# Optimization experiments

Measured on AMD Instinct MI355X. Metric: run time of the kernel, lower is better.

Reference implementation:

```python
import jax, jax.numpy as jnp
import numpy as np

D_MODEL, D_STATE, D_CONV, EXPAND = 1024, 16, 4, 2
D_INNER = D_MODEL * EXPAND
BATCH, SEQ = 2, 2048


def setup_inputs() -> dict:
    key = jax.random.key(0)
    ks = jax.random.split(key, 10)
    s = lambda d: 1.0 / np.sqrt(d)
    return {
        "x": jax.random.normal(ks[0], (BATCH, SEQ, D_MODEL), jnp.float32),
        "norm_w": jnp.ones((D_MODEL,), jnp.float32),
        "norm_b": jnp.zeros((D_MODEL,), jnp.float32),
        "W_in": jax.random.normal(ks[1], (2 * D_INNER, D_MODEL), jnp.float32) * s(D_MODEL),
        "conv_w": jax.random.normal(ks[2], (D_INNER, D_CONV), jnp.float32) * s(D_CONV),
        "conv_b": jnp.zeros((D_INNER,), jnp.float32),
        "W_dt": jax.random.normal(ks[3], (D_INNER, D_INNER), jnp.float32) * s(D_INNER),
        "b_dt": jnp.zeros((D_INNER,), jnp.float32),
        "W_B": jax.random.normal(ks[4], (D_STATE, D_INNER), jnp.float32) * s(D_INNER),
        "W_C": jax.random.normal(ks[5], (D_STATE, D_INNER), jnp.float32) * s(D_INNER),
        "D": jnp.ones((D_INNER,), jnp.float32),
        "A_log": jnp.broadcast_to(jnp.log(jnp.arange(1, D_STATE + 1, dtype=jnp.float32)), (D_INNER, D_STATE)),
        "W_out": jax.random.normal(ks[6], (D_MODEL, D_INNER), jnp.float32) * s(D_INNER),
    }


def _layernorm(x, w, b, eps=1e-5):
    mu = jnp.mean(x, axis=-1, keepdims=True)
    var = jnp.var(x, axis=-1, keepdims=True)
    return (x - mu) * jax.lax.rsqrt(var + eps) * w + b


def _causal_depthwise_conv(x, w, b):
    # x: [B, L, C], w: [C, K], b: [C]; torch Conv1d(padding=K-1) then slice [:L] == left-pad causal conv
    K = w.shape[1]
    xp = jnp.pad(x, ((0, 0), (K - 1, 0), (0, 0)))
    L = x.shape[1]
    out = b
    for k in range(K):  # small fixed K=4
        out = out + xp[:, k:k + L, :] * w[:, k]
    return out


def reference(x, norm_w, norm_b, W_in, conv_w, conv_b, W_dt, b_dt, W_B, W_C, D, A_log, W_out):
    residual = x
    xn = _layernorm(x, norm_w, norm_b)
    xz = jnp.einsum("bld,ed->ble", xn, W_in)            # [B,L,2*d_inner]
    x_part, z = jnp.split(xz, 2, axis=-1)
    x_conv = jax.nn.silu(_causal_depthwise_conv(x_part, conv_w, conv_b))  # [B,L,di]
    dt = jax.nn.softplus(jnp.einsum("bld,ed->ble", x_conv, W_dt) + b_dt)  # [B,L,di]
    Bm = jnp.einsum("bld,nd->bln", x_conv, W_B)         # [B,L,ds]
    Cm = jnp.einsum("bld,nd->bln", x_conv, W_C)         # [B,L,ds]
    A = -jnp.exp(A_log)                                  # [di,ds]

    def step(h, inp):
        dt_t, B_t, C_t, xc_t = inp                       # [B,di],[B,ds],[B,ds],[B,di]
        h = h * jnp.exp(A[None] * dt_t[:, :, None]) + xc_t[:, :, None] * B_t[:, None, :] * dt_t[:, :, None]
        y_t = jnp.sum(h * C_t[:, None, :], axis=-1)      # [B,di]
        return h, y_t

    h0 = jnp.zeros((x.shape[0], A.shape[0], A.shape[1]), x_conv.dtype)
    # scan over time: move L to leading axis
    xs = (jnp.swapaxes(dt, 0, 1), jnp.swapaxes(Bm, 0, 1), jnp.swapaxes(Cm, 0, 1), jnp.swapaxes(x_conv, 0, 1))
    _, y = jax.lax.scan(step, h0, xs)                    # y: [L,B,di]
    y = jnp.swapaxes(y, 0, 1)
    y = y + x_conv * D
    y = y * jax.nn.silu(z)
    return residual + jnp.einsum("ble,de->bld", y, W_out)
```

## Files before the change

kernel.cpp:

```cpp
#include <hip/hip_runtime.h>
#include <cstdint>
#include <cstddef>

#define D_MODEL 1024
#define D_INNER 2048
#define D_STATE 16
#define SEQ     2048
#define NROWS   4096

typedef short short4v __attribute__((ext_vector_type(4)));
typedef short short8v __attribute__((ext_vector_type(8)));
typedef float float4v __attribute__((ext_vector_type(4)));

__device__ __forceinline__ float bf2f(short u) {
  union { unsigned int i; float f; } v;
  v.i = ((unsigned int)(unsigned short)u) << 16;
  return v.f;
}
__device__ __forceinline__ short f2bf(float f) {
  union { float f; unsigned int i; } v; v.f = f;
  unsigned int r = v.i + 0x7FFFu + ((v.i >> 16) & 1u);
  return (short)(r >> 16);
}
__device__ __forceinline__ float lde(const void* p, size_t i, int f32) {
  return f32 ? ((const float*)p)[i] : bf2f(((const short*)p)[i]);
}
__device__ __forceinline__ void async16(short* lds, const short* g) {
  __builtin_amdgcn_global_load_lds(
      (const __attribute__((address_space(1))) unsigned int*)g,
      (__attribute__((address_space(3))) unsigned int*)lds, 16, 0, 0);
}

__global__ __launch_bounds__(64) void probe_kernel(const unsigned int* __restrict__ xw,
                                                   int* __restrict__ flag) {
  int cnt = 0;
  for (int i = threadIdx.x; i < 1024; i += 64) {
    unsigned e = (xw[i] >> 7) & 0xFFu;
    cnt += (e >= 100u && e <= 150u) ? 1 : 0;
  }
  #pragma unroll
  for (int o = 32; o >= 1; o >>= 1) cnt += __shfl_xor(cnt, o);
  if (threadIdx.x == 0) *flag = (cnt < 614) ? 1 : 0;
}

#define WIN_N  4194304u
#define WDT_N  4194304u
#define WBC_N  32768u
#define WPAD_N 196608u
#define WCAT_N (WDT_N + 2u*WBC_N + WPAD_N)
#define WOUT_N 2097152u
__global__ __launch_bounds__(256) void cvt_kernel(
    const void* __restrict__ Win, const void* __restrict__ Wdt,
    const void* __restrict__ WBp, const void* __restrict__ WCp,
    const void* __restrict__ Wout, short* __restrict__ dst,
    const int* __restrict__ flag) {
  const int f32 = *flag;
  const size_t i = ((size_t)blockIdx.x * 256 + threadIdx.x) * 8;
  const void* src = nullptr; size_t off = 0; bool zero = false;
  if (i < WIN_N) { src = Win; off = i; }
  else {
    size_t j = i - WIN_N;
    if (j < WDT_N) { src = Wdt; off = j; }
    else {
      j -= WDT_N;
      if (j < WBC_N) { src = WBp; off = j; }
      else {
        j -= WBC_N;
        if (j < WBC_N) { src = WCp; off = j; }
        else {
          j -= WBC_N;
          if (j < WPAD_N) zero = true;
          else { src = Wout; off = j - WPAD_N; }
        }
      }
    }
  }
  short8v o;
  if (zero) {
    #pragma unroll
    for (int j = 0; j < 8; ++j) o[j] = 0;
  } else if (f32) {
    const float* s = (const float*)src + off;
    #pragma unroll
    for (int j = 0; j < 8; ++j) o[j] = f2bf(s[j]);
  } else {
    o = *(const short8v*)((const short*)src + off);
  }
  *(short8v*)&dst[i] = o;
}

__global__ __launch_bounds__(256) void ln_kernel(
    const void* __restrict__ x, const void* __restrict__ w,
    const void* __restrict__ bb, short* __restrict__ xn,
    const int* __restrict__ flag) {
  const int f32 = *flag;
  const int row = blockIdx.x;
  const int tid = threadIdx.x;
  float v0, v1, v2, v3;
  if (f32) {
    float4v xv = ((const float4v*)((const float*)x + (size_t)row * D_MODEL))[tid];
    v0 = xv[0]; v1 = xv[1]; v2 = xv[2]; v3 = xv[3];
  } else {
    short4v xv = *(const short4v*)&((const short*)x)[(size_t)row * D_MODEL + tid * 4];
    v0 = bf2f(xv[0]); v1 = bf2f(xv[1]); v2 = bf2f(xv[2]); v3 = bf2f(xv[3]);
  }
  float s = v0 + v1 + v2 + v3;
  float q = v0*v0 + v1*v1 + v2*v2 + v3*v3;
  #pragma unroll
  for (int off = 32; off >= 1; off >>= 1) {
    s += __shfl_xor(s, off);
    q += __shfl_xor(q, off);
  }
  __shared__ float red[8];
  const int wid = tid >> 6;
  if ((tid & 63) == 0) { red[wid] = s; red[4 + wid] = q; }
  __syncthreads();
  s = red[0] + red[1] + red[2] + red[3];
  q = red[4] + red[5] + red[6] + red[7];
  const float mu = s * (1.f / 1024.f);
  const float var = q * (1.f / 1024.f) - mu * mu;
  const float rstd = rsqrtf(var + 1e-5f);
  short4v ov;
  #pragma unroll
  for (int j = 0; j < 4; ++j) {
    const float vj = (j == 0) ? v0 : (j == 1) ? v1 : (j == 2) ? v2 : v3;
    const float o = (vj - mu) * rstd * lde(w, tid * 4 + j, f32) + lde(bb, tid * 4 + j, f32);
    ov[j] = f2bf(o);
  }
  *(short4v*)&xn[(size_t)row * D_MODEL + tid * 4] = ov;
}

template <int MODE, int BM>
__global__ __launch_bounds__(2 * BM) void gemm_bt(
    const short* __restrict__ A, int lda, const short* __restrict__ B,
    void* __restrict__ Cv, int N, int K, const void* __restrict__ aux,
    float* __restrict__ Bmo, float* __restrict__ Cmo,
    const int* __restrict__ flag) {
  __shared__ __align__(16) short As0[BM * 32];
  __shared__ __align__(16) short As1[BM * 32];
  __shared__ __align__(16) short Bs0[128 * 32];
  __shared__ __align__(16) short Bs1[128 * 32];
  const int f32 = *flag;
  const int tid = threadIdx.x;
  const int bm = blockIdx.y * BM;
  const int bn = blockIdx.x << 7;
  const int wid = tid >> 6;
  const int lane = tid & 63;
  const int wm = (wid >> 1) << 6;
  const int wn = (wid & 1) << 6;

  float4v acc[4][4];
  #pragma unroll
  for (int i = 0; i < 4; ++i)
    #pragma unroll
    for (int j = 0; j < 4; ++j) acc[i][j] = (float4v){0.f, 0.f, 0.f, 0.f};

  const int srow = tid >> 2;
  const int scol = (((tid & 3) ^ ((tid >> 3) & 3)) << 3);
  const short* ga = A + (size_t)(bm + srow) * lda + scol;
  const short* gb = B + (size_t)(bn + srow) * K + scol;
  const size_t astep = (size_t)(BM / 2) * lda;
  const size_t bstep = (size_t)64 * K;

  const int fr = lane & 15;
  const int fq = (((lane >> 4) ^ ((lane >> 1) & 3)) << 3);

  constexpr int STAGE_DMAS = (BM == 256) ? 3 : 4;
  constexpr int VM_WAIT = 0x3FF0 | STAGE_DMAS;

#define STAGE(Ad, Bd, kk) do {                              \
    async16(&Ad[tid * 8], ga + (kk));                       \
    async16(&Ad[BM * 16 + tid * 8], ga + astep + (kk));     \
    if (BM == 256) {                                        \
      async16(&Bd[tid * 8], gb + (kk));                     \
    } else {                                                \
      async16(&Bd[tid * 8], gb + (kk));                     \
      async16(&Bd[2048 + tid * 8], gb + bstep + (kk));      \
    } } while (0)

  auto compute = [&](const short* Asrc, const short* Bsrc) {
    short8v af[4], bfv[4];
    #pragma unroll
    for (int i = 0; i < 4; ++i)
      af[i] = *(const short8v*)&Asrc[(wm + i * 16 + fr) * 32 + fq];
    #pragma unroll
    for (int j = 0; j < 4; ++j)
      bfv[j] = *(const short8v*)&Bsrc[(wn + j * 16 + fr) * 32 + fq];
    #pragma unroll
    for (int i = 0; i < 4; ++i)
      #pragma unroll
      for (int j = 0; j < 4; ++j)
        acc[i][j] = __builtin_amdgcn_mfma_f32_16x16x32_bf16(af[i], bfv[j], acc[i][j], 0, 0, 0);
  };

  const int nk = K >> 5;
  STAGE(As0, Bs0, 0);
  for (int k2 = 0; k2 < nk; k2 += 2) {
    STAGE(As1, Bs1, (k2 + 1) << 5);
    __builtin_amdgcn_s_waitcnt(VM_WAIT);
    __builtin_amdgcn_s_barrier();
    compute(As0, Bs0);
    __builtin_amdgcn_s_barrier();
    if (k2 + 2 < nk) {
      STAGE(As0, Bs0, (k2 + 2) << 5);
      __builtin_amdgcn_s_waitcnt(VM_WAIT);
    } else {
      __builtin_amdgcn_s_waitcnt(0x3FF0);
    }
    __builtin_amdgcn_s_barrier();
    compute(As1, Bs1);
    __builtin_amdgcn_s_barrier();
  }
#undef STAGE

  const int er = (lane >> 4) << 2;
  const int ec = lane & 15;
  #pragma unroll
  for (int i = 0; i < 4; ++i) {
    #pragma unroll
    for (int j = 0; j < 4; ++j) {
      const int gcol = bn + wn + j * 16 + ec;
      #pragma unroll
      for (int r = 0; r < 4; ++r) {
        const int grow = bm + wm + i * 16 + er + r;
        float v = acc[i][j][r];
        if (MODE == 1) {
          if (gcol < 2048) {
            v += lde(aux, gcol, f32);
            v = (v > 15.f) ? v : log1pf(__expf(v));
            ((short*)Cv)[(size_t)grow * 2048 + gcol] = f2bf(v);
          } else if (gcol < 2064) {
            Bmo[(size_t)grow * 16 + (gcol - 2048)] = v;
          } else if (gcol < 2080) {
            Cmo[(size_t)grow * 16 + (gcol - 2064)] = v;
          }
        } else {
          const size_t idx = (size_t)grow * N + gcol;
          if (MODE == 2) {
            v += lde(aux, idx, f32);
            if (f32) ((float*)Cv)[idx] = v;
            else     ((short*)Cv)[idx] = f2bf(v);
          } else {
            ((short*)Cv)[idx] = f2bf(v);
          }
        }
      }
    }
  }
}

__global__ __launch_bounds__(256) void bc_kernel(
    const short* __restrict__ xcv, const short* __restrict__ wbc,
    float* __restrict__ Bmo, float* __restrict__ Cmo) {
  const int tid = threadIdx.x;
  const int w = tid >> 6;
  const int lane = tid & 63;
  const int fr = lane & 15;
  const int hi = lane >> 4;
  const int r0 = blockIdx.x << 4;
  const short* ap  = xcv + (size_t)(r0 + fr) * 2048 + hi * 8;
  const short* b0p = wbc + (size_t)fr * 2048 + hi * 8;
  const short* b1p = wbc + (size_t)(16 + fr) * 2048 + hi * 8;
  float4v acc0 = (float4v){0.f, 0.f, 0.f, 0.f};
  float4v acc1 = (float4v){0.f, 0.f, 0.f, 0.f};
  #pragma unroll 4
  for (int k = w * 32; k < 2048; k += 128) {
    const short8v af  = *(const short8v*)(ap + k);
    const short8v bf0 = *(const short8v*)(b0p + k);
    const short8v bf1 = *(const short8v*)(b1p + k);
    acc0 = __builtin_amdgcn_mfma_f32_16x16x32_bf16(af, bf0, acc0, 0, 0, 0);
    acc1 = __builtin_amdgcn_mfma_f32_16x16x32_bf16(af, bf1, acc1, 0, 0, 0);
  }
  __shared__ float red[3][64][8];
  if (w) {
    #pragma unroll
    for (int r = 0; r < 4; ++r) {
      red[w - 1][lane][r]     = acc0[r];
      red[w - 1][lane][4 + r] = acc1[r];
    }
  }
  __syncthreads();
  if (w == 0) {
    #pragma unroll
    for (int c = 0; c < 3; ++c)
      #pragma unroll
      for (int r = 0; r < 4; ++r) {
        acc0[r] += red[c][lane][r];
        acc1[r] += red[c][lane][4 + r];
      }
    const int er = hi << 2;
    const int ec = fr;
    #pragma unroll
    for (int r = 0; r < 4; ++r) {
      Bmo[(size_t)(r0 + er + r) * 16 + ec] = acc0[r];
      Cmo[(size_t)(r0 + er + r) * 16 + ec] = acc1[r];
    }
  }
}

#define CONV_RPB 8
__global__ __launch_bounds__(256) void conv_silu(
    const short* __restrict__ xz, const void* __restrict__ cw,
    const void* __restrict__ cb, short* __restrict__ xc,
    const int* __restrict__ flag) {
  const int f32 = *flag;
  const int r0 = blockIdx.x * CONV_RPB;
  const int c0 = threadIdx.x << 3;
  const int t0 = r0 & (SEQ - 1);

  float wreg[32], bias[8];
  if (f32) {
    const float4v* wp = (const float4v*)((const float*)cw + (size_t)c0 * 4);
    #pragma unroll
    for (int q = 0; q < 8; ++q) {
      const float4v v = wp[q];
      #pragma unroll
      for (int k = 0; k < 4; ++k) wreg[q * 4 + k] = v[k];
    }
    const float4v* bp = (const float4v*)((const float*)cb + c0);
    const float4v b0 = bp[0], b1 = bp[1];
    #pragma unroll
    for (int j = 0; j < 4; ++j) { bias[j] = b0[j]; bias[4 + j] = b1[j]; }
  } else {
    const short8v* wp = (const short8v*)((const short*)cw + (size_t)c0 * 4);
    #pragma unroll
    for (int q = 0; q < 4; ++q) {
      const short8v v = wp[q];
      #pragma unroll
      for (int e = 0; e < 8; ++e) wreg[q * 8 + e] = bf2f(v[e]);
    }
    const short8v bv = *(const short8v*)((const short*)cb + c0);
    #pragma unroll
    for (int j = 0; j < 8; ++j) bias[j] = bf2f(bv[j]);
  }

  float xw[4][8];
  #pragma unroll
  for (int k = 0; k < 3; ++k) {
    if (t0 + k - 3 >= 0) {
      const short8v v = *(const short8v*)&xz[(size_t)(r0 + k - 3) * 4096 + c0];
      #pragma unroll
      for (int j = 0; j < 8; ++j) xw[k][j] = bf2f(v[j]);
    } else {
      #pragma unroll
      for (int j = 0; j < 8; ++j) xw[k][j] = 0.f;
    }
  }
  #pragma unroll
  for (int t = 0; t < CONV_RPB; ++t) {
    const int row = r0 + t;
    const short8v v = *(const short8v*)&xz[(size_t)row * 4096 + c0];
    #pragma unroll
    for (int j = 0; j < 8; ++j) xw[3][j] = bf2f(v[j]);
    short8v ov;
    #pragma unroll
    for (int j = 0; j < 8; ++j) {
      float a = bias[j];
      #pragma unroll
      for (int k = 0; k < 4; ++k) a += xw[k][j] * wreg[j * 4 + k];
      ov[j] = f2bf(a / (1.f + __expf(-a)));
    }
    *(short8v*)&xc[(size_t)row * D_INNER + c0] = ov;
    #pragma unroll
    for (int k = 0; k < 3; ++k)
      #pragma unroll
      for (int j = 0; j < 8; ++j) xw[k][j] = xw[k + 1][j];
  }
}

#define SCAN_CK 64
#define SCAN_ST 32
__global__ __launch_bounds__(1024, 4) void scan_kernel(
    const short* __restrict__ dtb, const short* __restrict__ xcv,
    const float* __restrict__ Bm, const float* __restrict__ Cm,
    short* __restrict__ xzb, const void* __restrict__ A_log,
    const void* __restrict__ Dv, const int* __restrict__ flag) {
  const int f32 = *flag;
  const int tid = threadIdx.x;
  const int dl = tid & 15;
  const int ck = tid >> 4;
  const int di = (blockIdx.x << 4) + dl;
  const int b = blockIdx.y;
  const int r0 = (b << 11) + ck * SCAN_ST;

  const short* dtp = dtb + (size_t)r0 * 2048 + di;
  const short* xcp = xcv + (size_t)r0 * 2048 + di;
  const float* bmp = Bm + (size_t)r0 * 16;
  const float* cmp = Cm + (size_t)r0 * 16;
  const short* zp = xzb + (size_t)r0 * 4096 + 2048 + di;
  short* yp = xzb + (size_t)r0 * 4096 + di;

  float Ac[16];
  #pragma unroll
  for (int s = 0; s < 16; ++s)
    Ac[s] = -__expf(lde(A_log, (size_t)di * 16 + s, f32));
  const float Dval = lde(Dv, di, f32);

  bool pat = true;
  #pragma unroll
  for (int s = 1; s < 16; ++s)
    pat = pat && (fabsf(Ac[s] - (float)(s + 1) * Ac[0]) <= fabsf(Ac[s]) * 1e-3f + 1e-6f);
  const float al = Ac[0] * 1.442695041f;

#define POWCHAIN(es, e1) do {                                        \
    es[0] = (e1);                                                    \
    es[1] = es[0] * es[0];  es[2] = es[1] * es[0];                   \
    es[3] = es[1] * es[1];  es[4] = es[3] * es[0];                   \
    es[5] = es[3] * es[1];  es[6] = es[3] * es[2];                   \
    es[7] = es[3] * es[3];  es[8] = es[7] * es[0];                   \
    es[9] = es[7] * es[1];  es[10] = es[7] * es[2];                  \
    es[11] = es[7] * es[3]; es[12] = es[7] * es[4];                  \
    es[13] = es[7] * es[5]; es[14] = es[7] * es[6];                  \
    es[15] = es[7] * es[7]; } while (0)

  float h[16];
  #pragma unroll
  for (int s = 0; s < 16; ++s) h[s] = 0.f;
  float sdt = 0.f;

  if (pat) {
    #pragma unroll 2
    for (int t = 0; t < SCAN_ST; ++t) {
      const float dt = bf2f(dtp[(size_t)t * 2048]);
      const float xc = bf2f(xcp[(size_t)t * 2048]);
      const float4v b0 = *(const float4v*)&bmp[t * 16];
      const float4v b1 = *(const float4v*)&bmp[t * 16 + 4];
      const float4v b2 = *(const float4v*)&bmp[t * 16 + 8];
      const float4v b3 = *(const float4v*)&bmp[t * 16 + 12];
      sdt += dt;
      const float u = xc * dt;
      float es[16];
      POWCHAIN(es, exp2f(al * dt));
      #pragma unroll
      for (int s = 0; s < 4; ++s) {
        h[s]      = h[s]      * es[s]      + u * b0[s];
        h[s + 4]  = h[s + 4]  * es[s + 4]  + u * b1[s];
        h[s + 8]  = h[s + 8]  * es[s + 8]  + u * b2[s];
        h[s + 12] = h[s + 12] * es[s + 12] + u * b3[s];
      }
    }
  } else {
    #pragma unroll 2
    for (int t = 0; t < SCAN_ST; ++t) {
      const float dt = bf2f(dtp[(size_t)t * 2048]);
      const float xc = bf2f(xcp[(size_t)t * 2048]);
      const float4v b0 = *(const float4v*)&bmp[t * 16];
      const float4v b1 = *(const float4v*)&bmp[t * 16 + 4];
      const float4v b2 = *(const float4v*)&bmp[t * 16 + 8];
      const float4v b3 = *(const float4v*)&bmp[t * 16 + 12];
      sdt += dt;
      const float u = xc * dt;
      #pragma unroll
      for (int s = 0; s < 4; ++s) {
        h[s]      = h[s]      * __expf(Ac[s]      * dt) + u * b0[s];
        h[s + 4]  = h[s + 4]  * __expf(Ac[s + 4]  * dt) + u * b1[s];
        h[s + 8]  = h[s + 8]  * __expf(Ac[s + 8]  * dt) + u * b2[s];
        h[s + 12] = h[s + 12] * __expf(Ac[s + 12] * dt) + u * b3[s];
      }
    }
  }

  __shared__ float sdt_s[SCAN_CK][16];
  __shared__ float hc_s[SCAN_CK][16][17];
  sdt_s[ck][dl] = sdt;
  #pragma unroll
  for (int s = 0; s < 16; ++s) hc_s[ck][dl][s] = h[s];
  __syncthreads();
  if (tid < 256) {
    const int s = tid >> 4;
    const float Acs = -__expf(lde(A_log, (size_t)di * 16 + s, f32));
    float hs = 0.f;
    #pragma unroll 4
    for (int c = 0; c < SCAN_CK; ++c) {
      const float hend = hc_s[c][dl][s];
      hc_s[c][dl][s] = hs;
      hs = __expf(Acs * sdt_s[c][dl]) * hs + hend;
    }
  }
  __syncthreads();
  #pragma unroll
  for (int s = 0; s < 16; ++s) h[s] = hc_s[ck][dl][s];

  if (pat) {
    #pragma unroll 2
    for (int t = 0; t < SCAN_ST; ++t) {
      const float dt = bf2f(dtp[(size_t)t * 2048]);
      const float xc = bf2f(xcp[(size_t)t * 2048]);
      const float4v b0 = *(const float4v*)&bmp[t * 16];
      const float4v b1 = *(const float4v*)&bmp[t * 16 + 4];
      const float4v b2 = *(const float4v*)&bmp[t * 16 + 8];
      const float4v b3 = *(const float4v*)&bmp[t * 16 + 12];
      const float4v c0 = *(const float4v*)&cmp[t * 16];
      const float4v c1 = *(const float4v*)&cmp[t * 16 + 4];
      const float4v c2 = *(const float4v*)&cmp[t * 16 + 8];
      const float4v c3 = *(const float4v*)&cmp[t * 16 + 12];
      const float u = xc * dt;
      float es[16];
      POWCHAIN(es, exp2f(al * dt));
      float p0 = 0.f, p1 = 0.f, p2 = 0.f, p3 = 0.f;
      #pragma unroll
      for (int s = 0; s < 4; ++s) {
        h[s]      = h[s]      * es[s]      + u * b0[s];
        h[s + 4]  = h[s + 4]  * es[s + 4]  + u * b1[s];
        h[s + 8]  = h[s + 8]  * es[s + 8]  + u * b2[s];
        h[s + 12] = h[s + 12] * es[s + 12] + u * b3[s];
        p0 += h[s] * c0[s];
        p1 += h[s + 4] * c1[s];
        p2 += h[s + 8] * c2[s];
        p3 += h[s + 12] * c3[s];
      }
      const float p = (p0 + p1) + (p2 + p3);
      const float z = bf2f(zp[(size_t)t * 4096]);
      const float sz = z * __builtin_amdgcn_rcpf(1.f + __expf(-z));
      yp[(size_t)t * 4096] = f2bf((p + xc * Dval) * sz);
    }
  } else {
    #pragma unroll 2
    for (int t = 0; t < SCAN_ST; ++t) {
      const float dt = bf2f(dtp[(size_t)t * 2048]);
      const float xc = bf2f(xcp[(size_t)t * 2048]);
      const float4v b0 = *(const float4v*)&bmp[t * 16];
      const float4v b1 = *(const float4v*)&bmp[t * 16 + 4];
      const float4v b2 = *(const float4v*)&bmp[t * 16 + 8];
      const float4v b3 = *(const float4v*)&bmp[t * 16 + 12];
      const float4v c0 = *(const float4v*)&cmp[t * 16];
      const float4v c1 = *(const float4v*)&cmp[t * 16 + 4];
      const float4v c2 = *(const float4v*)&cmp[t * 16 + 8];
      const float4v c3 = *(const float4v*)&cmp[t * 16 + 12];
      const float u = xc * dt;
      float p0 = 0.f, p1 = 0.f, p2 = 0.f, p3 = 0.f;
      #pragma unroll
      for (int s = 0; s < 4; ++s) {
        h[s]      = h[s]      * __expf(Ac[s]      * dt) + u * b0[s];
        h[s + 4]  = h[s + 4]  * __expf(Ac[s + 4]  * dt) + u * b1[s];
        h[s + 8]  = h[s + 8]  * __expf(Ac[s + 8]  * dt) + u * b2[s];
        h[s + 12] = h[s + 12] * __expf(Ac[s + 12] * dt) + u * b3[s];
        p0 += h[s] * c0[s];
        p1 += h[s + 4] * c1[s];
        p2 += h[s + 8] * c2[s];
        p3 += h[s + 12] * c3[s];
      }
      const float p = (p0 + p1) + (p2 + p3);
      const float z = bf2f(zp[(size_t)t * 4096]);
      const float sz = z * __builtin_amdgcn_rcpf(1.f + __expf(-z));
      yp[(size_t)t * 4096] = f2bf((p + xc * Dval) * sz);
    }
  }
#undef POWCHAIN
}

extern "C" void kernel_launch(void* const* d_in, const int* in_sizes, int n_in,
                              void* d_out, int out_size, void* d_ws, size_t ws_size,
                              hipStream_t stream) {
  const void* x      = d_in[0];
  const void* norm_w = d_in[1];
  const void* norm_b = d_in[2];
  const void* W_in   = d_in[3];
  const void* conv_w = d_in[4];
  const void* conv_b = d_in[5];
  const void* W_dt   = d_in[6];
  const void* b_dt   = d_in[7];
  const void* W_B    = d_in[8];
  const void* W_C    = d_in[9];
  const void* Dv     = d_in[10];
  const void* A_log  = d_in[11];
  const void* W_out  = d_in[12];

  char* ws = (char*)d_ws;
  const size_t MB = (size_t)1 << 20;
  short* wcvt = (short*)(ws);
  short* wbuf = wcvt;
  short* wcat = wcvt + WIN_N;
  short* wout = wcvt + WIN_N + WCAT_N;
  int*   flag = (int*)(ws + 21 * MB - 256);
  short* xzb  = (short*)(ws + 21 * MB);
  short* xcv  = (short*)(ws + 53 * MB);
  short* xn   = (short*)(ws + 69 * MB);
  short* dtb  = (short*)(ws + 69 * MB);
  float* Bm   = (float*)(ws + 85 * MB);
  float* Cm   = Bm + (size_t)NROWS * 16;

  probe_kernel<<<1, 64, 0, stream>>>((const unsigned int*)x, flag);
  cvt_kernel<<<5248, 256, 0, stream>>>(W_in, W_dt, W_B, W_C, W_out, wcvt, flag);
  ln_kernel<<<NROWS, 256, 0, stream>>>(x, norm_w, norm_b, xn, flag);
  gemm_bt<0, 256><<<dim3(32, 16), 512, 0, stream>>>(xn, 1024, wbuf, xzb, 4096, 1024, nullptr, nullptr, nullptr, flag);
  conv_silu<<<NROWS / CONV_RPB, 256, 0, stream>>>(xzb, conv_w, conv_b, xcv, flag);
  gemm_bt<1, 256><<<dim3(16, 16), 512, 0, stream>>>(xcv, 2048, wcat, dtb, 2176, 2048, b_dt, nullptr, nullptr, flag);
  bc_kernel<<<256, 256, 0, stream>>>(xcv, wcat + (size_t)2048 * 2048, Bm, Cm);
  scan_kernel<<<dim3(128, 2), 1024, 0, stream>>>(dtb, xcv, Bm, Cm, xzb, A_log, Dv, flag);
  gemm_bt<2, 128><<<dim3(8, 32), 256, 0, stream>>>(xzb, 4096, wout, d_out, 1024, 2048, x, nullptr, nullptr, flag);
}
```

Before: 396.4 us.

## Replace multi-wave GEMM with single-wave small-tile kernel and XCD-aware block remap

Replaces the 4/8-wave 256x128 block GEMM with a one-wave (64-thread) kernel computing 64x64 or 32x64 tiles. Inter-wave barriers go away in favour of waitcnt-only double buffering, and the block index is permuted so consecutive tiles land on the same XCD for L2 locality. The dt GEMM also drops the padded B/C columns, which the separate bc_kernel already produces. Smaller tiles mean much less operand reuse per block and more global/L2 traffic, in exchange for many more blocks and no barrier stalls.

```diff
diff --git a/kernel.cpp b/kernel.cpp
--- a/kernel.cpp
+++ b/kernel.cpp
@@ -131,27 +131,26 @@
 }
 
 template <int MODE, int BM>
-__global__ __launch_bounds__(2 * BM) void gemm_bt(
+__global__ __launch_bounds__(64) void gemm_w(
     const short* __restrict__ A, int lda, const short* __restrict__ B,
     void* __restrict__ Cv, int N, int K, const void* __restrict__ aux,
-    float* __restrict__ Bmo, float* __restrict__ Cmo,
     const int* __restrict__ flag) {
-  __shared__ __align__(16) short As0[BM * 32];
-  __shared__ __align__(16) short As1[BM * 32];
-  __shared__ __align__(16) short Bs0[128 * 32];
-  __shared__ __align__(16) short Bs1[128 * 32];
+  constexpr int RA = BM / 16;
+  __shared__ __align__(16) short As[2][BM * 32];
+  __shared__ __align__(16) short Bs[2][64 * 32];
   const int f32 = *flag;
   const int tid = threadIdx.x;
-  const int bm = blockIdx.y * BM;
-  const int bn = blockIdx.x << 7;
-  const int wid = tid >> 6;
-  const int lane = tid & 63;
-  const int wm = (wid >> 1) << 6;
-  const int wn = (wid & 1) << 6;
-
-  float4v acc[4][4];
-  #pragma unroll
-  for (int i = 0; i < 4; ++i)
+
+  const int gx = gridDim.x;
+  int lid = blockIdx.y * gx + blockIdx.x;
+  const int cpx = (gx * gridDim.y) >> 3;
+  lid = (lid & 7) * cpx + (lid >> 3);
+  const int bn = (lid % gx) << 6;
+  const int bm = (lid / gx) * BM;
+
+  float4v acc[RA][4];
+  #pragma unroll
+  for (int i = 0; i < RA; ++i)
     #pragma unroll
     for (int j = 0; j < 4; ++j) acc[i][j] = (float4v){0.f, 0.f, 0.f, 0.f};
 
@@ -159,81 +158,61 @@
   const int scol = (((tid & 3) ^ ((tid >> 3) & 3)) << 3);
   const short* ga = A + (size_t)(bm + srow) * lda + scol;
   const short* gb = B + (size_t)(bn + srow) * K + scol;
-  const size_t astep = (size_t)(BM / 2) * lda;
-  const size_t bstep = (size_t)64 * K;
-
-  const int fr = lane & 15;
-  const int fq = (((lane >> 4) ^ ((lane >> 1) & 3)) << 3);
-
-  constexpr int STAGE_DMAS = (BM == 256) ? 3 : 4;
-  constexpr int VM_WAIT = 0x3FF0 | STAGE_DMAS;
-
-#define STAGE(Ad, Bd, kk) do {                              \
-    async16(&Ad[tid * 8], ga + (kk));                       \
-    async16(&Ad[BM * 16 + tid * 8], ga + astep + (kk));     \
-    if (BM == 256) {                                        \
-      async16(&Bd[tid * 8], gb + (kk));                     \
-    } else {                                                \
-      async16(&Bd[tid * 8], gb + (kk));                     \
-      async16(&Bd[2048 + tid * 8], gb + bstep + (kk));      \
-    } } while (0)
-
-  auto compute = [&](const short* Asrc, const short* Bsrc) {
-    short8v af[4], bfv[4];
+
+  const int fr = tid & 15;
+  const int fq = (((tid >> 4) ^ ((tid >> 1) & 3)) << 3);
+
+  auto stage = [&](int buf, int kk) {
+    #pragma unroll
+    for (int i = 0; i < RA; ++i)
+      async16(&As[buf][i * 512 + tid * 8], ga + (size_t)(i * 16) * lda + kk);
     #pragma unroll
     for (int i = 0; i < 4; ++i)
-      af[i] = *(const short8v*)&Asrc[(wm + i * 16 + fr) * 32 + fq];
+      async16(&Bs[buf][i * 512 + tid * 8], gb + (size_t)(i * 16) * K + kk);
+  };
+  auto compute = [&](int buf) {
+    short8v af[RA], bfv[4];
+    #pragma unroll
+    for (int i = 0; i < RA; ++i)
+      af[i] = *(const short8v*)&As[buf][(i * 16 + fr) * 32 + fq];
     #pragma unroll
     for (int j = 0; j < 4; ++j)
-      bfv[j] = *(const short8v*)&Bsrc[(wn + j * 16 + fr) * 32 + fq];
-    #pragma unroll
-    for (int i = 0; i < 4; ++i)
+      bfv[j] = *(const short8v*)&Bs[buf][(j * 16 + fr) * 32 + fq];
+    #pragma unroll
+    for (int i = 0; i < RA; ++i)
       #pragma unroll
       for (int j = 0; j < 4; ++j)
         acc[i][j] = __builtin_amdgcn_mfma_f32_16x16x32_bf16(af[i], bfv[j], acc[i][j], 0, 0, 0);
   };
 
+#define VMW(NW) __builtin_amdgcn_s_waitcnt(0x3FF0 | (NW))
+#define LGKM0   __builtin_amdgcn_s_waitcnt(0xC07F)
+
   const int nk = K >> 5;
-  STAGE(As0, Bs0, 0);
-  for (int k2 = 0; k2 < nk; k2 += 2) {
-    STAGE(As1, Bs1, (k2 + 1) << 5);
-    __builtin_amdgcn_s_waitcnt(VM_WAIT);
-    __builtin_amdgcn_s_barrier();
-    compute(As0, Bs0);
-    __builtin_amdgcn_s_barrier();
-    if (k2 + 2 < nk) {
-      STAGE(As0, Bs0, (k2 + 2) << 5);
-      __builtin_amdgcn_s_waitcnt(VM_WAIT);
-    } else {
-      __builtin_amdgcn_s_waitcnt(0x3FF0);
-    }
-    __builtin_amdgcn_s_barrier();
-    compute(As1, Bs1);
-    __builtin_amdgcn_s_barrier();
-  }
-#undef STAGE
-
-  const int er = (lane >> 4) << 2;
-  const int ec = lane & 15;
-  #pragma unroll
-  for (int i = 0; i < 4; ++i) {
+  stage(0, 0);
+  for (int k = 0; k + 2 < nk; k += 2) {
+    stage(1, (k + 1) << 5); VMW(RA + 4); compute(0); LGKM0;
+    stage(0, (k + 2) << 5); VMW(RA + 4); compute(1); LGKM0;
+  }
+  stage(1, (nk - 1) << 5); VMW(RA + 4); compute(0); VMW(0); compute(1);
+#undef VMW
+#undef LGKM0
+
+  const int er = (tid >> 4) << 2;
+  const int ec = tid & 15;
+  #pragma unroll
+  for (int i = 0; i < RA; ++i) {
     #pragma unroll
     for (int j = 0; j < 4; ++j) {
-      const int gcol = bn + wn + j * 16 + ec;
+      const int gcol = bn + j * 16 + ec;
       #pragma unroll
       for (int r = 0; r < 4; ++r) {
-        const int grow = bm + wm + i * 16 + er + r;
+        const int grow = bm + i * 16 + er + r;
         float v = acc[i][j][r];
         if (MODE == 1) {
-          if (gcol < 2048) {
-            v += lde(aux, gcol, f32);
-            v = (v > 15.f) ? v : log1pf(__expf(v));
-            ((short*)Cv)[(size_t)grow * 2048 + gcol] = f2bf(v);
-          } else if (gcol < 2064) {
-            Bmo[(size_t)grow * 16 + (gcol - 2048)] = v;
-          } else if (gcol < 2080) {
-            Cmo[(size_t)grow * 16 + (gcol - 2064)] = v;
-          }
+          v += lde(aux, gcol, f32);
+          v = (v > 15.f) ? v : log1pf(__expf(v));
+          ((short*)Cv)[(size_t)grow * 2048 + gcol] = f2bf(v);
         } else {
           const size_t idx = (size_t)grow * N + gcol;
           if (MODE == 2) {
@@ -583,10 +562,10 @@
   probe_kernel<<<1, 64, 0, stream>>>((const unsigned int*)x, flag);
   cvt_kernel<<<5248, 256, 0, stream>>>(W_in, W_dt, W_B, W_C, W_out, wcvt, flag);
   ln_kernel<<<NROWS, 256, 0, stream>>>(x, norm_w, norm_b, xn, flag);
-  gemm_bt<0, 256><<<dim3(32, 16), 512, 0, stream>>>(xn, 1024, wbuf, xzb, 4096, 1024, nullptr, nullptr, nullptr, flag);
+  gemm_w<0, 64><<<dim3(64, 64), 64, 0, stream>>>(xn, 1024, wbuf, xzb, 4096, 1024, nullptr, flag);
   conv_silu<<<NROWS / CONV_RPB, 256, 0, stream>>>(xzb, conv_w, conv_b, xcv, flag);
-  gemm_bt<1, 256><<<dim3(16, 16), 512, 0, stream>>>(xcv, 2048, wcat, dtb, 2176, 2048, b_dt, nullptr, nullptr, flag);
+  gemm_w<1, 64><<<dim3(32, 64), 64, 0, stream>>>(xcv, 2048, wcat, dtb, 2048, 2048, b_dt, flag);
   bc_kernel<<<256, 256, 0, stream>>>(xcv, wcat + (size_t)2048 * 2048, Bm, Cm);
   scan_kernel<<<dim3(128, 2), 1024, 0, stream>>>(dtb, xcv, Bm, Cm, xzb, A_log, Dv, flag);
-  gemm_bt<2, 128><<<dim3(8, 32), 256, 0, stream>>>(xzb, 4096, wout, d_out, 1024, 2048, x, nullptr, nullptr, flag);
-}
+  gemm_w<2, 32><<<dim3(16, 128), 64, 0, stream>>>(xzb, 4096, wout, d_out, 1024, 2048, x, flag);
+}
```

After: 418.6 us. 1.06x slower.

## Shrink GEMM N-tile to BM/2, drop B/C columns from dt GEMM, remap scan blocks

Applied to the files above, without the earlier changes.

The GEMM template now uses an N tile of BM/2 instead of a fixed 128, so each block issues one B DMA per stage. The dt GEMM no longer pads to 2176 columns or writes B/C outputs, and it launches 128x64 tiles over a 32x32 grid. The out-projection GEMM grid doubles along N. Smaller tiles give more blocks on the CUs at the cost of lower per-block MFMA reuse. The scan kernel becomes a 1D grid with a swizzled block-to-(channel,batch) mapping, intended to spread work across XCDs for cache locality.

```diff
diff --git a/kernel.cpp b/kernel.cpp
--- a/kernel.cpp
+++ b/kernel.cpp
@@ -134,106 +134,96 @@
 __global__ __launch_bounds__(2 * BM) void gemm_bt(
     const short* __restrict__ A, int lda, const short* __restrict__ B,
     void* __restrict__ Cv, int N, int K, const void* __restrict__ aux,
-    float* __restrict__ Bmo, float* __restrict__ Cmo,
     const int* __restrict__ flag) {
-  __shared__ __align__(16) short As0[BM * 32];
-  __shared__ __align__(16) short As1[BM * 32];
-  __shared__ __align__(16) short Bs0[128 * 32];
-  __shared__ __align__(16) short Bs1[128 * 32];
+  constexpr int BN = BM / 2;
+  constexpr int WNT = BN / 2;
+  constexpr int NJ = WNT / 16;
+  __shared__ __align__(16) short As[2][BM * 32];
+  __shared__ __align__(16) short Bs[2][BN * 32];
   const int f32 = *flag;
   const int tid = threadIdx.x;
   const int bm = blockIdx.y * BM;
-  const int bn = blockIdx.x << 7;
+  const int bn = blockIdx.x * BN;
   const int wid = tid >> 6;
   const int lane = tid & 63;
   const int wm = (wid >> 1) << 6;
-  const int wn = (wid & 1) << 6;
-
-  float4v acc[4][4];
+  const int wn = (wid & 1) * WNT;
+
+  float4v acc[4][NJ];
   #pragma unroll
   for (int i = 0; i < 4; ++i)
     #pragma unroll
-    for (int j = 0; j < 4; ++j) acc[i][j] = (float4v){0.f, 0.f, 0.f, 0.f};
+    for (int j = 0; j < NJ; ++j) acc[i][j] = (float4v){0.f, 0.f, 0.f, 0.f};
 
   const int srow = tid >> 2;
   const int scol = (((tid & 3) ^ ((tid >> 3) & 3)) << 3);
   const short* ga = A + (size_t)(bm + srow) * lda + scol;
   const short* gb = B + (size_t)(bn + srow) * K + scol;
   const size_t astep = (size_t)(BM / 2) * lda;
-  const size_t bstep = (size_t)64 * K;
 
   const int fr = lane & 15;
   const int fq = (((lane >> 4) ^ ((lane >> 1) & 3)) << 3);
 
-  constexpr int STAGE_DMAS = (BM == 256) ? 3 : 4;
-  constexpr int VM_WAIT = 0x3FF0 | STAGE_DMAS;
-
-#define STAGE(Ad, Bd, kk) do {                              \
-    async16(&Ad[tid * 8], ga + (kk));                       \
-    async16(&Ad[BM * 16 + tid * 8], ga + astep + (kk));     \
-    if (BM == 256) {                                        \
-      async16(&Bd[tid * 8], gb + (kk));                     \
-    } else {                                                \
-      async16(&Bd[tid * 8], gb + (kk));                     \
-      async16(&Bd[2048 + tid * 8], gb + bstep + (kk));      \
-    } } while (0)
-
-  auto compute = [&](const short* Asrc, const short* Bsrc) {
-    short8v af[4], bfv[4];
+#define STAGE(buf, kk) do {                                 \
+    async16(&As[buf][tid * 8], ga + (kk));                  \
+    async16(&As[buf][BM * 16 + tid * 8], ga + astep + (kk));\
+    async16(&Bs[buf][tid * 8], gb + (kk));                  \
+  } while (0)
+#define VMW(NW) __builtin_amdgcn_s_waitcnt(0x3FF0 | (NW))
+#define BAR __builtin_amdgcn_s_barrier()
+
+  auto compute = [&](int buf) {
+    short8v af[4], bfv[NJ];
     #pragma unroll
     for (int i = 0; i < 4; ++i)
-      af[i] = *(const short8v*)&Asrc[(wm + i * 16 + fr) * 32 + fq];
-    #pragma unroll
-    for (int j = 0; j < 4; ++j)
-      bfv[j] = *(const short8v*)&Bsrc[(wn + j * 16 + fr) * 32 + fq];
+      af[i] = *(const short8v*)&As[buf][(wm + i * 16 + fr) * 32 + fq];
+    #pragma unroll
+    for (int j = 0; j < NJ; ++j)
+      bfv[j] = *(const short8v*)&Bs[buf][(wn + j * 16 + fr) * 32 + fq];
     #pragma unroll
     for (int i = 0; i < 4; ++i)
       #pragma unroll
-      for (int j = 0; j < 4; ++j)
+      for (int j = 0; j < NJ; ++j)
         acc[i][j] = __builtin_amdgcn_mfma_f32_16x16x32_bf16(af[i], bfv[j], acc[i][j], 0, 0, 0);
   };
 
   const int nk = K >> 5;
-  STAGE(As0, Bs0, 0);
+  STAGE(0, 0);
   for (int k2 = 0; k2 < nk; k2 += 2) {
-    STAGE(As1, Bs1, (k2 + 1) << 5);
-    __builtin_amdgcn_s_waitcnt(VM_WAIT);
-    __builtin_amdgcn_s_barrier();
-    compute(As0, Bs0);
-    __builtin_amdgcn_s_barrier();
+    STAGE(1, (k2 + 1) << 5);
+    VMW(3);
+    BAR;
+    compute(0);
+    BAR;
     if (k2 + 2 < nk) {
-      STAGE(As0, Bs0, (k2 + 2) << 5);
-      __builtin_amdgcn_s_waitcnt(VM_WAIT);
+      STAGE(0, (k2 + 2) << 5);
+      VMW(3);
     } else {
-      __builtin_amdgcn_s_waitcnt(0x3FF0);
-    }
-    __builtin_amdgcn_s_barrier();
-    compute(As1, Bs1);
-    __builtin_amdgcn_s_barrier();
+      VMW(0);
+    }
+    BAR;
+    compute(1);
+    BAR;
   }
 #undef STAGE
+#undef VMW
+#undef BAR
 
   const int er = (lane >> 4) << 2;
   const int ec = lane & 15;
   #pragma unroll
   for (int i = 0; i < 4; ++i) {
     #pragma unroll
-    for (int j = 0; j < 4; ++j) {
+    for (int j = 0; j < NJ; ++j) {
       const int gcol = bn + wn + j * 16 + ec;
       #pragma unroll
       for (int r = 0; r < 4; ++r) {
         const int grow = bm + wm + i * 16 + er + r;
         float v = acc[i][j][r];
         if (MODE == 1) {
-          if (gcol < 2048) {
-            v += lde(aux, gcol, f32);
-            v = (v > 15.f) ? v : log1pf(__expf(v));
-            ((short*)Cv)[(size_t)grow * 2048 + gcol] = f2bf(v);
-          } else if (gcol < 2064) {
-            Bmo[(size_t)grow * 16 + (gcol - 2048)] = v;
-          } else if (gcol < 2080) {
-            Cmo[(size_t)grow * 16 + (gcol - 2064)] = v;
-          }
+          v += lde(aux, gcol, f32);
+          v = (v > 15.f) ? v : log1pf(__expf(v));
+          ((short*)Cv)[(size_t)grow * 2048 + gcol] = f2bf(v);
         } else {
           const size_t idx = (size_t)grow * N + gcol;
           if (MODE == 2) {
@@ -379,8 +369,11 @@
   const int tid = threadIdx.x;
   const int dl = tid & 15;
   const int ck = tid >> 4;
-  const int di = (blockIdx.x << 4) + dl;
-  const int b = blockIdx.y;
+  const int d = blockIdx.x;
+  const int s_ = ((d & 7) << 5) | (d >> 3);
+  const int bx = s_ & 127;
+  const int b = s_ >> 7;
+  const int di = (bx << 4) + dl;
   const int r0 = (b << 11) + ck * SCAN_ST;
 
   const short* dtp = dtb + (size_t)r0 * 2048 + di;
@@ -583,10 +576,10 @@
   probe_kernel<<<1, 64, 0, stream>>>((const unsigned int*)x, flag);
   cvt_kernel<<<5248, 256, 0, stream>>>(W_in, W_dt, W_B, W_C, W_out, wcvt, flag);
   ln_kernel<<<NROWS, 256, 0, stream>>>(x, norm_w, norm_b, xn, flag);
-  gemm_bt<0, 256><<<dim3(32, 16), 512, 0, stream>>>(xn, 1024, wbuf, xzb, 4096, 1024, nullptr, nullptr, nullptr, flag);
+  gemm_bt<0, 256><<<dim3(32, 16), 512, 0, stream>>>(xn, 1024, wbuf, xzb, 4096, 1024, nullptr, flag);
   conv_silu<<<NROWS / CONV_RPB, 256, 0, stream>>>(xzb, conv_w, conv_b, xcv, flag);
-  gemm_bt<1, 256><<<dim3(16, 16), 512, 0, stream>>>(xcv, 2048, wcat, dtb, 2176, 2048, b_dt, nullptr, nullptr, flag);
+  gemm_bt<1, 128><<<dim3(32, 32), 256, 0, stream>>>(xcv, 2048, wcat, dtb, 2048, 2048, b_dt, flag);
   bc_kernel<<<256, 256, 0, stream>>>(xcv, wcat + (size_t)2048 * 2048, Bm, Cm);
-  scan_kernel<<<dim3(128, 2), 1024, 0, stream>>>(dtb, xcv, Bm, Cm, xzb, A_log, Dv, flag);
-  gemm_bt<2, 128><<<dim3(8, 32), 256, 0, stream>>>(xzb, 4096, wout, d_out, 1024, 2048, x, nullptr, nullptr, flag);
-}
+  scan_kernel<<<256, 1024, 0, stream>>>(dtb, xcv, Bm, Cm, xzb, A_log, Dv, flag);
+  gemm_bt<2, 128><<<dim3(16, 32), 256, 0, stream>>>(xzb, 4096, wout, d_out, 1024, 2048, x, flag);
+}
```

New measurement: 381.2 us. -3.8%, faster.
